# Optimization experiments

Measured on AMD Instinct MI355X. Metric: run time of the kernel, lower is better.

Reference implementation:

```python
import jax, jax.numpy as jnp
import numpy as np

HID, DSTATE, K, DIN, HDIM, NH, CHUNK = 2048, 128, 4, 4096, 64, 64, 256
CONVD = DIN + 2 * DSTATE  # 4352
EPS = 1e-5


def setup_inputs() -> dict:
    key = jax.random.key(0)
    ks = jax.random.split(key, 10)
    B, L = 2, 4096
    hidden_states = jax.random.normal(ks[0], (B, L, HID), jnp.float32)
    proj_out = 2 * (DIN + DSTATE) + NH  # 8512
    in_proj_w = jax.random.normal(ks[1], (proj_out, HID), jnp.float32) * (HID ** -0.5)
    conv_w = jax.random.normal(ks[2], (CONVD, K), jnp.float32) * (K ** -0.5)
    conv_b = jax.random.normal(ks[3], (CONVD,), jnp.float32) * 0.01
    dt_bias = jax.random.uniform(ks[4], (NH,), jnp.float32)
    A = jax.random.uniform(ks[5], (NH,), jnp.float32, minval=1.0, maxval=16.0)
    A_log = jnp.log(A)
    D = jnp.ones((NH,), jnp.float32)
    norm_w = jnp.ones((DIN,), jnp.float32)
    out_proj_w = jax.random.normal(ks[6], (HID, DIN), jnp.float32) * (DIN ** -0.5)
    return {"hidden_states": hidden_states, "in_proj_w": in_proj_w, "conv_w": conv_w,
            "conv_b": conv_b, "dt_bias": dt_bias, "A_log": A_log, "D": D,
            "norm_w": norm_w, "out_proj_w": out_proj_w}


def _segsum(x):
    # x: [..., L] -> [..., L, L] lower-triangular cumulative sums, -inf above diag
    Lc = x.shape[-1]
    cs = jnp.cumsum(x, -1)
    seg = cs[..., :, None] - cs[..., None, :]
    mask = jnp.tril(jnp.ones((Lc, Lc), bool))
    return jnp.where(mask, seg, -jnp.inf)


def _causal_conv1d(x, w, b):
    # x: [B, L, D] depthwise causal conv, kernel K, then SiLU
    L = x.shape[1]
    xp = jnp.pad(x, ((0, 0), (K - 1, 0), (0, 0)))
    y = sum(xp[:, i:i + L, :] * w[:, i] for i in range(K)) + b
    return jax.nn.silu(y)


def _ssd(x, Bm, Cm, dt, A, D):
    # x:[b,l,h,p]  Bm,Cm:[b,l,n]  dt:[b,l,h] (post-softplus)  A:[h]  D:[h]
    b, l, h, p = x.shape
    n = Bm.shape[-1]
    c = l // CHUNK
    xr = x.reshape(b, c, CHUNK, h, p)
    Br = Bm.reshape(b, c, CHUNK, n)
    Cr = Cm.reshape(b, c, CHUNK, n)
    dtr = dt.reshape(b, c, CHUNK, h)
    Adt = jnp.transpose(dtr * A, (0, 3, 1, 2))          # [b,h,c,L]
    Acs = jnp.cumsum(Adt, -1)                            # [b,h,c,L]
    Lmat = jnp.exp(_segsum(Adt))                         # [b,h,c,L,L]
    xdt = xr * dtr[..., None]                            # [b,c,L,h,p]
    # intra-chunk (diagonal) term
    Yd = jnp.einsum('bcln,bcsn,bhcls,bcshp->bclhp', Cr, Br, Lmat, xdt)
    # per-chunk final states
    decay_states = jnp.exp(Acs[..., -1:] - Acs)          # [b,h,c,L]
    chunk_states = jnp.einsum('bcln,bhcl,bclhp->bchpn', Br, decay_states, xdt)
    chunk_decay = jnp.exp(Acs[..., -1])                  # [b,h,c]
    def step(state, inp):
        dec, cs = inp
        return state * dec[..., None, None] + cs, state
    init = jnp.zeros((b, h, p, n), x.dtype)
    _, prev = jax.lax.scan(step, init,
                           (jnp.moveaxis(chunk_decay, -1, 0), jnp.moveaxis(chunk_states, 1, 0)))
    prev = jnp.moveaxis(prev, 0, 1)                      # [b,c,h,p,n] state entering each chunk
    Yo = jnp.einsum('bcln,bchpn,bhcl->bclhp', Cr, prev, jnp.exp(Acs))
    Y = Yd + Yo + xr * D[:, None]
    return Y.reshape(b, l, h * p)


def _gated_rmsnorm(y, z, w):
    y32 = y.astype(jnp.float32) * jax.nn.silu(z.astype(jnp.float32))
    var = jnp.mean(y32 * y32, -1, keepdims=True)
    return (y32 * jax.lax.rsqrt(var + EPS) * w).astype(y.dtype)


def reference(hidden_states, in_proj_w, conv_w, conv_b, dt_bias, A_log, D, norm_w, out_proj_w):
    zxbcdt = hidden_states @ in_proj_w.T                 # [b,l,8512]
    z = zxbcdt[..., :DIN]
    xBC = zxbcdt[..., DIN:DIN + CONVD]
    dt = zxbcdt[..., DIN + CONVD:]                       # [b,l,h]
    xBC = _causal_conv1d(xBC, conv_w, conv_b)
    x = xBC[..., :DIN]
    Bm = xBC[..., DIN:DIN + DSTATE]
    Cm = xBC[..., DIN + DSTATE:]
    A = -jnp.exp(A_log)
    dt = jax.nn.softplus(dt + dt_bias)
    b, l, _ = x.shape
    y = _ssd(x.reshape(b, l, NH, HDIM), Bm, Cm, dt, A, D)
    y = _gated_rmsnorm(y, z, norm_w)
    return y @ out_proj_w.T
```

## Files before the change

kernel.cpp:

```cpp
#include <hip/hip_runtime.h>
#include <hip/hip_bf16.h>


typedef __bf16 v8bf __attribute__((ext_vector_type(8)));
typedef float  v4f  __attribute__((ext_vector_type(4)));

#define LL long long

__device__ inline v8bf load8(const float* p) {
    v4f a = *(const v4f*)p, b = *(const v4f*)(p + 4);
    v8bf r;
#pragma unroll
    for (int i = 0; i < 4; ++i) { r[i] = (__bf16)a[i]; r[i + 4] = (__bf16)b[i]; }
    return r;
}

__device__ __forceinline__ void gload_lds16(const __bf16* g, __bf16* l) {
    __builtin_amdgcn_global_load_lds(
        (const __attribute__((address_space(1))) void*)g,
        (__attribute__((address_space(3))) void*)l, 16, 0, 0);
}

__global__ __launch_bounds__(256) void cast_bf16_kernel(
    const float* __restrict__ in, __bf16* __restrict__ out)
{
    LL i = ((LL)blockIdx.x * 256 + threadIdx.x) * 8;
    *(v8bf*)&out[i] = load8(&in[i]);
}

__global__ __launch_bounds__(256) void cast_split_kernel(
    const float* __restrict__ in, __bf16* __restrict__ hi,
    __bf16* __restrict__ lo)
{
    LL i = ((LL)blockIdx.x * 256 + threadIdx.x) * 8;
    v4f a = *(const v4f*)&in[i], b = *(const v4f*)&in[i + 4];
    v8bf h, l;
#pragma unroll
    for (int k = 0; k < 4; ++k) {
        __bf16 hh = (__bf16)a[k];  h[k]     = hh;  l[k]     = (__bf16)(a[k] - (float)hh);
        __bf16 hb = (__bf16)b[k];  h[k + 4] = hb;  l[k + 4] = (__bf16)(b[k] - (float)hb);
    }
    *(v8bf*)&hi[i] = h;
    *(v8bf*)&lo[i] = l;
}

template <int MODE, int TM, int TN, int RN>
__global__ __launch_bounds__(512, 2) void gemm_bt_8p(
    const __bf16* __restrict__ Ab, const __bf16* __restrict__ Bb, int KT,
    int lda, int ldb,
    __bf16* __restrict__ z_out, __bf16* __restrict__ x_out,
    float* __restrict__ outf, int ldc)
{
    __shared__ __align__(16) __bf16 lds[65536];
    constexpr int RM = 8 / RN;
    constexpr int LM = TM / RM, LN = TN / RN;
    const int orig = blockIdx.x;
    const int x = orig & 7, loc = orig >> 3;
    const int M0 = ((x / RN) * LM + loc / LN) * 256;
    const int N0 = ((x % RN) * LN + loc % LN) * 256;

    const int tid  = threadIdx.x;
    const int lane = tid & 63, wave = tid >> 6;
    const int wr = wave >> 2, wc = wave & 3;
    const int lrow = lane & 15, quad = lane >> 4;
    const int row0 = tid >> 3;
    const int g0   = (tid & 7) ^ (row0 & 7);

    v4f acc[8][4] = {};
    v8bf aF[2][4], b0F[2][2], b1F[2][2];

#define STAGE_A(par, half, kt) do { \
    const __bf16* _s = Ab + (size_t)(M0 + (half)*128 + row0) * lda + (kt)*64 + g0*8; \
    __bf16* _d = lds + ((par)*2 + (half)) * 8192 + wave * 512; \
    gload_lds16(_s, _d); \
    gload_lds16(_s + (size_t)64 * lda, _d + 4096); \
} while (0)

#define STAGE_B(par, half, kt) do { \
    const __bf16* _s = Bb + (size_t)(N0 + (half)*128 + row0) * ldb + (kt)*64 + g0*8; \
    __bf16* _d = lds + 32768 + ((par)*2 + (half)) * 8192 + wave * 512; \
    gload_lds16(_s, _d); \
    gload_lds16(_s + (size_t)64 * ldb, _d + 4096); \
} while (0)

#define READ_A(par, qm) do { \
    const __bf16* _s = lds + ((par)*2 + wr) * 8192; \
    _Pragma("unroll") \
    for (int _ks = 0; _ks < 2; ++_ks) \
      _Pragma("unroll") \
      for (int _m = 0; _m < 4; ++_m) \
        aF[_ks][_m] = *(const v8bf*)&_s[((qm)*64 + _m*16 + lrow)*64 + \
                                        ((((_ks<<2)+quad) ^ (lrow&7))<<3)]; \
} while (0)

#define READ_B(par, qn, DST) do { \
    const __bf16* _s = lds + 32768 + ((par)*2 + (wc>>1)) * 8192; \
    _Pragma("unroll") \
    for (int _ks = 0; _ks < 2; ++_ks) \
      _Pragma("unroll") \
      for (int _n = 0; _n < 2; ++_n) \
        DST[_ks][_n] = *(const v8bf*)&_s[((wc&1)*64 + (qn)*32 + _n*16 + lrow)*64 + \
                                         ((((_ks<<2)+quad) ^ (lrow&7))<<3)]; \
} while (0)

#define MFQ(qm, qn, BF) do { \
    __builtin_amdgcn_s_setprio(1); \
    _Pragma("unroll") \
    for (int _ks = 0; _ks < 2; ++_ks) \
      _Pragma("unroll") \
      for (int _m = 0; _m < 4; ++_m) \
        _Pragma("unroll") \
        for (int _n = 0; _n < 2; ++_n) \
          acc[(qm)*4+_m][(qn)*2+_n] = __builtin_amdgcn_mfma_f32_16x16x32_bf16( \
              aF[_ks][_m], BF[_ks][_n], acc[(qm)*4+_m][(qn)*2+_n], 0, 0, 0); \
    __builtin_amdgcn_s_setprio(0); \
} while (0)

#define PBAR  __builtin_amdgcn_s_barrier()
#define LGKM0 asm volatile("s_waitcnt lgkmcnt(0)" ::: "memory")
#define VMC4  asm volatile("s_waitcnt vmcnt(4)" ::: "memory")
#define VMC0  asm volatile("s_waitcnt vmcnt(0)" ::: "memory")

    STAGE_A(0, 0, 0); STAGE_A(0, 1, 0); STAGE_B(0, 0, 0); STAGE_B(0, 1, 0);
    STAGE_A(1, 0, 1); STAGE_B(1, 0, 1);
    VMC4; PBAR;

    const int KT2 = KT >> 1;
    for (int it = 0; it < KT2; ++it) {
        const int T0 = 2 * it, T1 = 2 * it + 1;
        const bool notlast = (it < KT2 - 1);
        READ_A(0, 0); READ_B(0, 0, b0F);
        STAGE_A(1, 1, T1);
        PBAR; LGKM0; MFQ(0, 0, b0F); PBAR;
        READ_B(0, 1, b1F);
        STAGE_B(1, 1, T1);
        PBAR; LGKM0; MFQ(0, 1, b1F); PBAR;
        READ_A(0, 1);
        if (notlast) STAGE_B(0, 0, T0 + 2);
        PBAR; LGKM0; MFQ(1, 0, b0F); PBAR;
        if (notlast) STAGE_A(0, 0, T0 + 2);
        PBAR; LGKM0; MFQ(1, 1, b1F);
        if (notlast) { VMC4; } else { VMC0; }
        PBAR;
        READ_A(1, 0); READ_B(1, 0, b0F);
        if (notlast) STAGE_A(0, 1, T0 + 2);
        PBAR; LGKM0; MFQ(0, 0, b0F); PBAR;
        READ_B(1, 1, b1F);
        if (notlast) STAGE_B(0, 1, T0 + 2);
        PBAR; LGKM0; MFQ(0, 1, b1F); PBAR;
        READ_A(1, 1);
        if (notlast) STAGE_B(1, 0, T1 + 2);
        PBAR; LGKM0; MFQ(1, 0, b0F); PBAR;
        if (notlast) STAGE_A(1, 0, T1 + 2);
        PBAR; LGKM0; MFQ(1, 1, b1F);
        if (notlast) { VMC4; } else { VMC0; }
        PBAR;
    }

#undef STAGE_A
#undef STAGE_B
#undef READ_A
#undef READ_B
#undef MFQ

#pragma unroll
    for (int m = 0; m < 8; ++m)
#pragma unroll
        for (int n = 0; n < 4; ++n)
#pragma unroll
            for (int r = 0; r < 4; ++r) {
                int row = M0 + wr * 128 + m * 16 + quad * 4 + r;
                int col = N0 + wc * 64 + n * 16 + lrow;
                float v = acc[m][n][r];
                if constexpr (MODE == 1) {
                    if (col < 4096) z_out[(LL)row * 4096 + col] = (__bf16)v;
                    else            x_out[(LL)row * 4096 + (col - 4096)] = (__bf16)v;
                } else {
                    outf[(LL)row * ldc + col] = v;
                }
            }
}

__global__ __launch_bounds__(256) void bcdt_gemm_kernel(
    const __bf16* __restrict__ Ahi, const __bf16* __restrict__ Alo,
    const __bf16* __restrict__ Whi, const __bf16* __restrict__ Wlo,
    const float* __restrict__ dtbi,
    float* __restrict__ bcr, float* __restrict__ dt)
{
    __shared__ __align__(16) __bf16 sAh[128 * 64];
    __shared__ __align__(16) __bf16 sAl[128 * 64];
    __shared__ __align__(16) __bf16 sWh[64 * 64];
    __shared__ __align__(16) __bf16 sWl[64 * 64];
    const int orig = blockIdx.x;
    const int swz = (orig & 7) * 40 + (orig >> 3);
    const int m0 = (swz / 5) * 128;
    const int n0 = (swz % 5) * 64;
    const int tid = threadIdx.x;
    const int lane = tid & 63, wave = tid >> 6;
    const int lrow = lane & 15, quad = lane >> 4;
    const int wm = wave * 32;
    v4f acc[2][4] = {};

    for (int k0 = 0; k0 < 2048; k0 += 64) {
#pragma unroll
        for (int i = 0; i < 4; ++i) {
            int e = tid + i * 256;
            int row = e >> 3, g = (e & 7) ^ (row & 7);
            const LL so = (LL)(m0 + row) * 2048 + k0 + g * 8;
            gload_lds16(&Ahi[so], &sAh[wave * 512 + i * 2048]);
            gload_lds16(&Alo[so], &sAl[wave * 512 + i * 2048]);
        }
#pragma unroll
        for (int i = 0; i < 2; ++i) {
            int e = tid + i * 256;
            int row = e >> 3, g = (e & 7) ^ (row & 7);
            const LL so = (LL)(n0 + row) * 2048 + k0 + g * 8;
            gload_lds16(&Whi[so], &sWh[wave * 512 + i * 2048]);
            gload_lds16(&Wlo[so], &sWl[wave * 512 + i * 2048]);
        }
        __syncthreads();
#pragma unroll
        for (int ks = 0; ks < 2; ++ks) {
            v8bf ah[2], al[2], wh[4], wl[4];
#pragma unroll
            for (int i = 0; i < 2; ++i) {
                int r = wm + i * 16 + lrow;
                int c = ((((ks << 2) + quad) ^ (lrow & 7)) << 3);
                ah[i] = *(const v8bf*)&sAh[r * 64 + c];
                al[i] = *(const v8bf*)&sAl[r * 64 + c];
            }
#pragma unroll
            for (int j = 0; j < 4; ++j) {
                int r = j * 16 + lrow;
                int c = ((((ks << 2) + quad) ^ (lrow & 7)) << 3);
                wh[j] = *(const v8bf*)&sWh[r * 64 + c];
                wl[j] = *(const v8bf*)&sWl[r * 64 + c];
            }
#pragma unroll
            for (int i = 0; i < 2; ++i)
#pragma unroll
                for (int j = 0; j < 4; ++j) {
                    acc[i][j] = __builtin_amdgcn_mfma_f32_16x16x32_bf16(ah[i], wh[j], acc[i][j], 0, 0, 0);
                    acc[i][j] = __builtin_amdgcn_mfma_f32_16x16x32_bf16(ah[i], wl[j], acc[i][j], 0, 0, 0);
                    acc[i][j] = __builtin_amdgcn_mfma_f32_16x16x32_bf16(al[i], wh[j], acc[i][j], 0, 0, 0);
                }
        }
        __syncthreads();
    }
#pragma unroll
    for (int i = 0; i < 2; ++i)
#pragma unroll
        for (int j = 0; j < 4; ++j)
#pragma unroll
            for (int r = 0; r < 4; ++r) {
                int row = m0 + wm + i * 16 + quad * 4 + r;
                int sc = n0 + j * 16 + lrow;
                float v = acc[i][j][r];
                if (sc < 256) {
                    bcr[(LL)row * 256 + sc] = v;
                } else {
                    float x = v + dtbi[sc - 256];
                    dt[row * 64 + (sc - 256)] = (x > 20.f) ? x : log1pf(__expf(x));
                }
            }
}

__global__ __launch_bounds__(256) void conv_x_kernel(
    const __bf16* __restrict__ xp, const float* __restrict__ cw,
    const float* __restrict__ cbias, __bf16* __restrict__ xq)
{
    int ch = blockIdx.x * 256 + threadIdx.x;
    int l = blockIdx.y, b = blockIdx.z;
    float acc = cbias[ch];
#pragma unroll
    for (int i = 0; i < 4; ++i) {
        int ls = l - 3 + i;
        if (ls >= 0)
            acc += (float)xp[((LL)b * 4096 + ls) * 4096 + ch] * cw[ch * 4 + i];
    }
    acc = acc / (1.f + __expf(-acc));
    xq[((LL)b * 4096 + l) * 4096 + ch] = (__bf16)acc;
}

__global__ __launch_bounds__(256) void conv_bc_kernel(
    const float* __restrict__ bcr, const float* __restrict__ cw,
    const float* __restrict__ cbias, float* __restrict__ bcc)
{
    int ch = threadIdx.x;
    int l = blockIdx.y, b = blockIdx.z;
    float acc = cbias[4096 + ch];
#pragma unroll
    for (int i = 0; i < 4; ++i) {
        int ls = l - 3 + i;
        if (ls >= 0)
            acc += bcr[((LL)b * 4096 + ls) * 256 + ch] * cw[(4096 + ch) * 4 + i];
    }
    acc = acc / (1.f + __expf(-acc));
    bcc[((LL)b * 4096 + l) * 256 + ch] = acc;
}

__global__ __launch_bounds__(256) void cumsum_kernel(
    const float* __restrict__ dt, const float* __restrict__ alog,
    float* __restrict__ acs, float* __restrict__ cdec)
{
    int h = blockIdx.x, c = blockIdx.y, b = blockIdx.z;
    int s = threadIdx.x;
    __shared__ float buf[256];
    float Av = -expf(alog[h]);
    int bl = b * 4096 + c * 256 + s;
    buf[s] = dt[bl * 64 + h] * Av;
    __syncthreads();
    for (int off = 1; off < 256; off <<= 1) {
        float v = (s >= off) ? buf[s - off] : 0.f;
        __syncthreads();
        buf[s] += v;
        __syncthreads();
    }
    int abase = (((b * 16) + c) * 64 + h) * 256;
    acs[abase + s] = buf[s];
    if (s == 255) cdec[(b * 64 + h) * 16 + c] = expf(buf[s]);
}

__global__ __launch_bounds__(256) void chunk_state_kernel(
    const __bf16* __restrict__ xq, const float* __restrict__ bcc,
    const float* __restrict__ dtb, const float* __restrict__ acs,
    float* __restrict__ cs)
{
    int h = blockIdx.x, c = blockIdx.y, b = blockIdx.z;
    int t = threadIdx.x;
    int lg = t & 63, pg = t >> 6;
    int n0 = lg * 2;
    __shared__ __align__(16) float xdt_s[64 * 68];
    __shared__ float dec_s[64];
    const LL lbase = (LL)b * 4096 + c * 256;
    const int abase = (((b * 16) + c) * 64 + h) * 256;
    float alast = acs[abase + 255];
    float a0[16] = {}, a1[16] = {};
    for (int st = 0; st < 4; ++st) {
        for (int i = 0; i < 16; ++i) {
            int e = t + i * 256; int sp = e >> 6, p = e & 63;
            LL row = lbase + st * 64 + sp;
            xdt_s[sp * 68 + p] = (float)xq[row * 4096 + h * 64 + p] * dtb[(row << 6) + h];
        }
        if (t < 64) dec_s[t] = __expf(alast - acs[abase + st * 64 + t]);
        __syncthreads();
        for (int sp = 0; sp < 64; ++sp) {
            LL row = lbase + st * 64 + sp;
            float2 bb = *(const float2*)&bcc[row * 256 + n0];
            float dd = dec_s[sp];
            float b0 = bb.x * dd, b1 = bb.y * dd;
#pragma unroll
            for (int q = 0; q < 4; ++q) {
                v4f xv = *(const v4f*)&xdt_s[sp * 68 + pg * 16 + q * 4];
#pragma unroll
                for (int j = 0; j < 4; ++j) { a0[q * 4 + j] += b0 * xv[j]; a1[q * 4 + j] += b1 * xv[j]; }
            }
        }
        __syncthreads();
    }
    const LL obase = ((LL)(((b * 16) + c) * 64 + h)) * 8192;
    for (int pp = 0; pp < 16; ++pp) {
        int p = pg * 16 + pp;
        cs[obase + p * 128 + n0]     = a0[pp];
        cs[obase + p * 128 + n0 + 1] = a1[pp];
    }
}

__global__ __launch_bounds__(256) void scan_kernel(
    float* __restrict__ cs, const float* __restrict__ cdec)
{
    int h = blockIdx.x, b = blockIdx.y;
    int t = threadIdx.x;
    float st[32];
#pragma unroll
    for (int i = 0; i < 32; ++i) st[i] = 0.f;
    for (int c = 0; c < 16; ++c) {
        LL base = ((LL)(((b * 16) + c) * 64 + h)) * 8192;
        float cd = cdec[(b * 64 + h) * 16 + c];
#pragma unroll
        for (int i = 0; i < 32; ++i) {
            int e = i * 256 + t;
            float v = cs[base + e];
            cs[base + e] = st[i];
            st[i] = st[i] * cd + v;
        }
    }
}

__global__ __launch_bounds__(256) void cb_kernel(const float* __restrict__ bcc,
                                                 float* __restrict__ cbt)
{
    int st = blockIdx.x, c = blockIdx.y, b = blockIdx.z;
    int t = threadIdx.x;
    int lg = t & 63, pg = t >> 6;
    __shared__ float cr_s[256 * 33];
    __shared__ __align__(16) float brT[32 * 68];
    const LL lbase = (LL)b * 4096 + c * 256;
    float acc[4][16] = {};
    for (int nt = 0; nt < 4; ++nt) {
        for (int i = 0; i < 32; ++i) {
            int e = t + i * 256; int l = e >> 5, np = e & 31;
            cr_s[l * 33 + np] = bcc[(lbase + l) * 256 + 128 + nt * 32 + np];
        }
        for (int i = 0; i < 8; ++i) {
            int e = t + i * 256; int sp = e >> 5, np = e & 31;
            brT[np * 68 + sp] = bcc[(lbase + st * 64 + sp) * 256 + nt * 32 + np];
        }
        __syncthreads();
        for (int np = 0; np < 32; ++np) {
            float w0 = cr_s[lg * 33 + np],         w1 = cr_s[(lg + 64) * 33 + np];
            float w2 = cr_s[(lg + 128) * 33 + np], w3 = cr_s[(lg + 192) * 33 + np];
#pragma unroll
            for (int q = 0; q < 4; ++q) {
                v4f bv = *(const v4f*)&brT[np * 68 + pg * 16 + q * 4];
#pragma unroll
                for (int j = 0; j < 4; ++j) {
                    acc[0][q * 4 + j] += w0 * bv[j]; acc[1][q * 4 + j] += w1 * bv[j];
                    acc[2][q * 4 + j] += w2 * bv[j]; acc[3][q * 4 + j] += w3 * bv[j];
                }
            }
        }
        __syncthreads();
    }
    const LL obase = ((LL)((b * 16) + c)) * 65536;
#pragma unroll
    for (int r = 0; r < 4; ++r)
        for (int sp = 0; sp < 16; ++sp) {
            int s = st * 64 + pg * 16 + sp;
            cbt[obase + (LL)s * 256 + (lg + r * 64)] = acc[r][sp];
        }
}

__global__ __launch_bounds__(256) void ssd_y_kernel(
    __bf16* __restrict__ xq, const float* __restrict__ bcc,
    const float* __restrict__ dtb, const float* __restrict__ acs,
    const float* __restrict__ cbt, const float* __restrict__ prevS,
    const float* __restrict__ Dv)
{
    const int h = blockIdx.x, c = blockIdx.y, b = blockIdx.z;
    const int t = threadIdx.x;
    const int lane = t & 63, wave = t >> 6;
    const int lrow = lane & 15, quad = lane >> 4;
    const int wm = wave * 64;
    __shared__ __align__(16) __bf16 As[256][72];
    __shared__ __align__(16) __bf16 Bs[64 * 64];
    __shared__ float acs_s[256];
    const LL lbase = (LL)b * 4096 + c * 256;
    const int abase = (((b * 16) + c) * 64 + h) * 256;
    acs_s[t] = acs[abase + t];
    __syncthreads();
    const float acl_t = acs_s[t];
    const float ea_t  = __expf(acl_t);
    const LL cbbase = ((LL)((b * 16) + c)) * 65536;
    const LL pbase  = ((LL)(((b * 16) + c) * 64 + h)) * 8192;
    v4f acc[4][4] = {};

    for (int kb = 0; kb < 6; ++kb) {
        if (kb < 4) {
            const int sb = kb * 64;
#pragma unroll
            for (int g = 0; g < 8; ++g) {
                v8bf wv;
#pragma unroll
                for (int u = 0; u < 8; ++u) {
                    int s = sb + g * 8 + u;
                    float cbv = cbt[cbbase + (LL)s * 256 + t];
                    float d = acl_t - acs_s[s];
                    wv[u] = (__bf16)((s <= t) ? cbv * __expf(d) : 0.f);
                }
                *(v8bf*)&As[t][g * 8] = wv;
            }
        } else {
            const int nb = (kb - 4) * 64;
            const LL cb0 = (lbase + t) * 256 + 128 + nb;
#pragma unroll
            for (int g = 0; g < 8; ++g) {
                v4f c0 = *(const v4f*)&bcc[cb0 + g * 8];
                v4f c1 = *(const v4f*)&bcc[cb0 + g * 8 + 4];
                v8bf wv;
#pragma unroll
                for (int u = 0; u < 4; ++u) {
                    wv[u]     = (__bf16)(c0[u] * ea_t);
                    wv[u + 4] = (__bf16)(c1[u] * ea_t);
                }
                *(v8bf*)&As[t][g * 8] = wv;
            }
        }
        if (kb < 4) {
            const int sb = kb * 64;
#pragma unroll
            for (int i = 0; i < 16; ++i) {
                int e = t + i * 256; int p = e & 63, sp = e >> 6;
                LL row = lbase + sb + sp;
                float xv = (float)xq[row * 4096 + h * 64 + p] * dtb[((int)(row)) * 64 + h];
                Bs[p * 64 + ((((sp >> 3) ^ (p & 7)) << 3) | (sp & 7))] = (__bf16)xv;
            }
        } else {
            const int nb = (kb - 4) * 64;
#pragma unroll
            for (int i = 0; i < 16; ++i) {
                int e = t + i * 256; int n = e & 63, p = e >> 6;
                float pv = prevS[pbase + (LL)p * 128 + nb + n];
                Bs[p * 64 + ((((n >> 3) ^ (p & 7)) << 3) | (n & 7))] = (__bf16)pv;
            }
        }
        __syncthreads();
#pragma unroll
        for (int ks = 0; ks < 2; ++ks) {
            v8bf af[4], bfv[4];
#pragma unroll
            for (int i = 0; i < 4; ++i)
                af[i] = *(const v8bf*)&As[wm + i * 16 + lrow][ks * 32 + quad * 8];
#pragma unroll
            for (int j = 0; j < 4; ++j) {
                int p = j * 16 + lrow;
                int kg = (ks * 4 + quad) ^ (p & 7);
                bfv[j] = *(const v8bf*)&Bs[p * 64 + kg * 8];
            }
#pragma unroll
            for (int i = 0; i < 4; ++i)
#pragma unroll
                for (int j = 0; j < 4; ++j)
                    acc[i][j] = __builtin_amdgcn_mfma_f32_16x16x32_bf16(af[i], bfv[j], acc[i][j], 0, 0, 0);
        }
        __syncthreads();
    }
    const float Dh = Dv[h];
#pragma unroll
    for (int i = 0; i < 4; ++i)
#pragma unroll
        for (int j = 0; j < 4; ++j)
#pragma unroll
            for (int r = 0; r < 4; ++r) {
                int l = wm + i * 16 + quad * 4 + r;
                int p = j * 16 + lrow;
                LL idx = (lbase + l) * 4096 + h * 64 + p;
                float v = acc[i][j][r] + Dh * (float)xq[idx];
                xq[idx] = (__bf16)v;
            }
}

__global__ __launch_bounds__(256) void rmsnorm_kernel(
    __bf16* __restrict__ y, const __bf16* __restrict__ z,
    const float* __restrict__ nw)
{
    LL r = blockIdx.x;
    int t = threadIdx.x;
    float vals[16]; float ss = 0.f;
#pragma unroll
    for (int i = 0; i < 16; ++i) {
        int j = i * 256 + t;
        float yv = (float)y[r * 4096 + j];
        float zv = (float)z[r * 4096 + j];
        float v = yv * (zv / (1.f + __expf(-zv)));
        vals[i] = v; ss += v * v;
    }
#pragma unroll
    for (int off = 32; off >= 1; off >>= 1) ss += __shfl_down(ss, off, 64);
    __shared__ float red[4];
    if ((t & 63) == 0) red[t >> 6] = ss;
    __syncthreads();
    float tot = red[0] + red[1] + red[2] + red[3];
    float rstd = rsqrtf(tot * (1.f / 4096.f) + 1e-5f);
#pragma unroll
    for (int i = 0; i < 16; ++i) {
        int j = i * 256 + t;
        y[r * 4096 + j] = (__bf16)(vals[i] * rstd * nw[j]);
    }
}

extern "C" void kernel_launch(void* const* d_in, const int* in_sizes, int n_in,
                              void* d_out, int out_size, void* d_ws, size_t ws_size,
                              hipStream_t stream) {
    const float* hs    = (const float*)d_in[0];
    const float* w1    = (const float*)d_in[1];
    const float* cw    = (const float*)d_in[2];
    const float* cbias = (const float*)d_in[3];
    const float* dtbi  = (const float*)d_in[4];
    const float* alog  = (const float*)d_in[5];
    const float* Dv    = (const float*)d_in[6];
    const float* nw    = (const float*)d_in[7];
    const float* wo    = (const float*)d_in[8];
    float* out = (float*)d_out;
    (void)in_sizes; (void)n_in; (void)out_size; (void)ws_size;

    char* ws = (char*)d_ws;
    size_t off = 0;
    auto alloc = [&](size_t bytes) { void* p = ws + off; off += (bytes + 255) & ~(size_t)255; return p; };
    __bf16* xp_b  = (__bf16*)alloc((size_t)8192 * 4096 * 2);
    __bf16* xq_b  = (__bf16*)alloc((size_t)8192 * 4096 * 2);
    float*  bcr_f = (float*) alloc((size_t)8192 * 256 * 4);
    float*  bcc_f = (float*) alloc((size_t)8192 * 256 * 4);
    float*  dt_f  = (float*) alloc((size_t)8192 * 64 * 4);
    float*  acs_f = (float*) alloc((size_t)2 * 16 * 64 * 256 * 4);
    float*  cd_f  = (float*) alloc((size_t)2 * 64 * 16 * 4);
    float*  cbt_f = (float*) alloc((size_t)2 * 16 * 256 * 256 * 4);
    float*  cs_f  = (float*)xp_b;
    __bf16* z_b   = (__bf16*)d_out;

    __bf16* hs_b  = xq_b;
    __bf16* w1_b  = xq_b + (size_t)8192 * 2048;
    __bf16* hs_lo = (__bf16*)xp_b;
    __bf16* ws_hi = hs_lo + (size_t)8192 * 2048;
    __bf16* ws_lo = ws_hi + (size_t)320 * 2048;
    __bf16* wo_b  = (__bf16*)xp_b;

    cast_split_kernel<<<8192, 256, 0, stream>>>(hs, hs_b, hs_lo);
    cast_bf16_kernel<<<8192, 256, 0, stream>>>(w1, w1_b);
    cast_split_kernel<<<320, 256, 0, stream>>>(w1 + (size_t)8192 * 2048, ws_hi, ws_lo);
    bcdt_gemm_kernel<<<320, 256, 0, stream>>>(hs_b, hs_lo, ws_hi, ws_lo,
                                              dtbi, bcr_f, dt_f);
    gemm_bt_8p<1, 32, 32, 4><<<dim3(1024), 512, 0, stream>>>(
        hs_b, w1_b, 32, 2048, 2048, z_b, xp_b, nullptr, 0);
    conv_x_kernel<<<dim3(16, 4096, 2), 256, 0, stream>>>(xp_b, cw, cbias, xq_b);
    conv_bc_kernel<<<dim3(1, 4096, 2), 256, 0, stream>>>(bcr_f, cw, cbias, bcc_f);
    cumsum_kernel<<<dim3(64, 16, 2), 256, 0, stream>>>(dt_f, alog, acs_f, cd_f);
    chunk_state_kernel<<<dim3(64, 16, 2), 256, 0, stream>>>(xq_b, bcc_f, dt_f, acs_f, cs_f);
    scan_kernel<<<dim3(64, 2), 256, 0, stream>>>(cs_f, cd_f);
    cb_kernel<<<dim3(4, 16, 2), 256, 0, stream>>>(bcc_f, cbt_f);
    ssd_y_kernel<<<dim3(64, 16, 2), 256, 0, stream>>>(xq_b, bcc_f, dt_f, acs_f, cbt_f, cs_f, Dv);
    cast_bf16_kernel<<<4096, 256, 0, stream>>>(wo, wo_b);
    rmsnorm_kernel<<<8192, 256, 0, stream>>>(xq_b, z_b, nw);
    gemm_bt_8p<2, 32, 8, 1><<<dim3(256), 512, 0, stream>>>(
        xq_b, wo_b, 64, 4096, 4096, nullptr, nullptr, out, 2048);
}
```

Measured before the change: 1.389 ms.

## Skip causal-zero tiles in SSD diag term and split CB kernel rows

The intra-chunk term of the SSD output kernel now skips MFMA work for waves whose row block lies entirely above the causal diagonal. Off-diagonal tiles get their decay weights from a factored exp (row factor times a per-column factor in shared memory) instead of one exp per element, so only diagonal tiles compute full pairwise exps. The C-scaling fill is remapped to coalesced loads through a shared exp buffer. The CB kernel is split into twice as many blocks, each covering half the rows, to raise parallelism. In exchange the code adds more branching and an explicit waitcnt/sched barrier, and the factored exp may slightly change rounding.

```diff
diff --git a/kernel.cpp b/kernel.cpp
--- a/kernel.cpp
+++ b/kernel.cpp
@@ -390,17 +390,20 @@
 __global__ __launch_bounds__(256) void cb_kernel(const float* __restrict__ bcc,
                                                  float* __restrict__ cbt)
 {
-    int st = blockIdx.x, c = blockIdx.y, b = blockIdx.z;
+    int bx = blockIdx.x;
+    int st = bx & 3, lh = bx >> 2;
+    int c = blockIdx.y, b = blockIdx.z;
     int t = threadIdx.x;
     int lg = t & 63, pg = t >> 6;
-    __shared__ float cr_s[256 * 33];
+    __shared__ float cr_s[128 * 33];
     __shared__ __align__(16) float brT[32 * 68];
     const LL lbase = (LL)b * 4096 + c * 256;
-    float acc[4][16] = {};
+    const int l0 = lh * 128;
+    float acc[2][16] = {};
     for (int nt = 0; nt < 4; ++nt) {
-        for (int i = 0; i < 32; ++i) {
+        for (int i = 0; i < 16; ++i) {
             int e = t + i * 256; int l = e >> 5, np = e & 31;
-            cr_s[l * 33 + np] = bcc[(lbase + l) * 256 + 128 + nt * 32 + np];
+            cr_s[l * 33 + np] = bcc[(lbase + l0 + l) * 256 + 128 + nt * 32 + np];
         }
         for (int i = 0; i < 8; ++i) {
             int e = t + i * 256; int sp = e >> 5, np = e & 31;
@@ -408,15 +411,14 @@
         }
         __syncthreads();
         for (int np = 0; np < 32; ++np) {
-            float w0 = cr_s[lg * 33 + np],         w1 = cr_s[(lg + 64) * 33 + np];
-            float w2 = cr_s[(lg + 128) * 33 + np], w3 = cr_s[(lg + 192) * 33 + np];
+            float w0 = cr_s[lg * 33 + np], w1 = cr_s[(lg + 64) * 33 + np];
 #pragma unroll
             for (int q = 0; q < 4; ++q) {
                 v4f bv = *(const v4f*)&brT[np * 68 + pg * 16 + q * 4];
 #pragma unroll
                 for (int j = 0; j < 4; ++j) {
-                    acc[0][q * 4 + j] += w0 * bv[j]; acc[1][q * 4 + j] += w1 * bv[j];
-                    acc[2][q * 4 + j] += w2 * bv[j]; acc[3][q * 4 + j] += w3 * bv[j];
+                    acc[0][q * 4 + j] += w0 * bv[j];
+                    acc[1][q * 4 + j] += w1 * bv[j];
                 }
             }
         }
@@ -424,10 +426,10 @@
     }
     const LL obase = ((LL)((b * 16) + c)) * 65536;
 #pragma unroll
-    for (int r = 0; r < 4; ++r)
+    for (int r = 0; r < 2; ++r)
         for (int sp = 0; sp < 16; ++sp) {
             int s = st * 64 + pg * 16 + sp;
-            cbt[obase + (LL)s * 256 + (lg + r * 64)] = acc[r][sp];
+            cbt[obase + (LL)s * 256 + (l0 + lg + r * 64)] = acc[r][sp];
         }
 }
 
@@ -445,12 +447,14 @@
     __shared__ __align__(16) __bf16 As[256][72];
     __shared__ __align__(16) __bf16 Bs[64 * 64];
     __shared__ float acs_s[256];
+    __shared__ float ea_s[256];
+    __shared__ float qbuf[64];
     const LL lbase = (LL)b * 4096 + c * 256;
     const int abase = (((b * 16) + c) * 64 + h) * 256;
     acs_s[t] = acs[abase + t];
+    const float acl_t = acs_s[t];
+    ea_s[t] = __expf(acl_t);
     __syncthreads();
-    const float acl_t = acs_s[t];
-    const float ea_t  = __expf(acl_t);
     const LL cbbase = ((LL)((b * 16) + c)) * 65536;
     const LL pbase  = ((LL)(((b * 16) + c) * 64 + h)) * 8192;
     v4f acc[4][4] = {};
@@ -458,45 +462,49 @@
     for (int kb = 0; kb < 6; ++kb) {
         if (kb < 4) {
             const int sb = kb * 64;
-#pragma unroll
-            for (int g = 0; g < 8; ++g) {
-                v8bf wv;
-#pragma unroll
-                for (int u = 0; u < 8; ++u) {
-                    int s = sb + g * 8 + u;
-                    float cbv = cbt[cbbase + (LL)s * 256 + t];
-                    float d = acl_t - acs_s[s];
-                    wv[u] = (__bf16)((s <= t) ? cbv * __expf(d) : 0.f);
-                }
-                *(v8bf*)&As[t][g * 8] = wv;
-            }
-        } else {
-            const int nb = (kb - 4) * 64;
-            const LL cb0 = (lbase + t) * 256 + 128 + nb;
-#pragma unroll
-            for (int g = 0; g < 8; ++g) {
-                v4f c0 = *(const v4f*)&bcc[cb0 + g * 8];
-                v4f c1 = *(const v4f*)&bcc[cb0 + g * 8 + 4];
-                v8bf wv;
-#pragma unroll
-                for (int u = 0; u < 4; ++u) {
-                    wv[u]     = (__bf16)(c0[u] * ea_t);
-                    wv[u + 4] = (__bf16)(c1[u] * ea_t);
-                }
-                *(v8bf*)&As[t][g * 8] = wv;
-            }
-        }
-        if (kb < 4) {
-            const int sb = kb * 64;
+            if (t < 64) qbuf[t] = __expf(acs_s[sb + 63] - acs_s[sb + t]);
+            {
+                const int row = sb + wave * 16 + lrow;
+                const int c0 = quad * 16;
+                const float al = acs_s[row];
+                v8bf wv0, wv1;
+#pragma unroll
+                for (int j = 0; j < 8; ++j) {
+                    int s0 = sb + c0 + j;
+                    int s1 = s0 + 8;
+                    float cb0 = cbt[cbbase + (LL)s0 * 256 + row];
+                    float cb1 = cbt[cbbase + (LL)s1 * 256 + row];
+                    wv0[j] = (__bf16)((s0 <= row) ? cb0 * __expf(al - acs_s[s0]) : 0.f);
+                    wv1[j] = (__bf16)((s1 <= row) ? cb1 * __expf(al - acs_s[s1]) : 0.f);
+                }
+                *(v8bf*)&As[row][c0]     = wv0;
+                *(v8bf*)&As[row][c0 + 8] = wv1;
+            }
 #pragma unroll
             for (int i = 0; i < 16; ++i) {
                 int e = t + i * 256; int p = e & 63, sp = e >> 6;
                 LL row = lbase + sb + sp;
-                float xv = (float)xq[row * 4096 + h * 64 + p] * dtb[((int)(row)) * 64 + h];
+                float xv = (float)xq[row * 4096 + h * 64 + p] * dtb[((int)row) * 64 + h];
                 Bs[p * 64 + ((((sp >> 3) ^ (p & 7)) << 3) | (sp & 7))] = (__bf16)xv;
             }
         } else {
             const int nb = (kb - 4) * 64;
+#pragma unroll
+            for (int i = 0; i < 8; ++i) {
+                int e = t + i * 256;
+                int l = e >> 3, g = e & 7;
+                const LL cb0 = (lbase + l) * 256 + 128 + nb + g * 8;
+                v4f c0 = *(const v4f*)&bcc[cb0];
+                v4f c1 = *(const v4f*)&bcc[cb0 + 4];
+                float ea = ea_s[l];
+                v8bf wv;
+#pragma unroll
+                for (int u = 0; u < 4; ++u) {
+                    wv[u]     = (__bf16)(c0[u] * ea);
+                    wv[u + 4] = (__bf16)(c1[u] * ea);
+                }
+                *(v8bf*)&As[l][g * 8] = wv;
+            }
 #pragma unroll
             for (int i = 0; i < 16; ++i) {
                 int e = t + i * 256; int n = e & 63, p = e >> 6;
@@ -505,23 +513,45 @@
             }
         }
         __syncthreads();
-#pragma unroll
-        for (int ks = 0; ks < 2; ++ks) {
-            v8bf af[4], bfv[4];
-#pragma unroll
-            for (int i = 0; i < 4; ++i)
-                af[i] = *(const v8bf*)&As[wm + i * 16 + lrow][ks * 32 + quad * 8];
-#pragma unroll
-            for (int j = 0; j < 4; ++j) {
-                int p = j * 16 + lrow;
-                int kg = (ks * 4 + quad) ^ (p & 7);
-                bfv[j] = *(const v8bf*)&Bs[p * 64 + kg * 8];
-            }
-#pragma unroll
-            for (int i = 0; i < 4; ++i)
-#pragma unroll
-                for (int j = 0; j < 4; ++j)
-                    acc[i][j] = __builtin_amdgcn_mfma_f32_16x16x32_bf16(af[i], bfv[j], acc[i][j], 0, 0, 0);
+        if (kb < 4 && wave > kb) {
+            const int sb = kb * 64;
+            const float r = __expf(acl_t - acs_s[sb + 63]);
+#pragma unroll
+            for (int g = 0; g < 8; ++g) {
+                v4f q0 = *(const v4f*)&qbuf[g * 8];
+                v4f q1 = *(const v4f*)&qbuf[g * 8 + 4];
+                v8bf wv;
+#pragma unroll
+                for (int u = 0; u < 4; ++u) {
+                    float cbv0 = cbt[cbbase + (LL)(sb + g * 8 + u) * 256 + t];
+                    float cbv1 = cbt[cbbase + (LL)(sb + g * 8 + 4 + u) * 256 + t];
+                    wv[u]     = (__bf16)(cbv0 * (r * q0[u]));
+                    wv[u + 4] = (__bf16)(cbv1 * (r * q1[u]));
+                }
+                *(v8bf*)&As[t][g * 8] = wv;
+            }
+            asm volatile("s_waitcnt lgkmcnt(0)" ::: "memory");
+            __builtin_amdgcn_sched_barrier(0);
+        }
+        if (kb >= 4 || wave >= kb) {
+#pragma unroll
+            for (int ks = 0; ks < 2; ++ks) {
+                v8bf af[4], bfv[4];
+#pragma unroll
+                for (int i = 0; i < 4; ++i)
+                    af[i] = *(const v8bf*)&As[wm + i * 16 + lrow][ks * 32 + quad * 8];
+#pragma unroll
+                for (int j = 0; j < 4; ++j) {
+                    int p = j * 16 + lrow;
+                    int kg = (ks * 4 + quad) ^ (p & 7);
+                    bfv[j] = *(const v8bf*)&Bs[p * 64 + kg * 8];
+                }
+#pragma unroll
+                for (int i = 0; i < 4; ++i)
+#pragma unroll
+                    for (int j = 0; j < 4; ++j)
+                        acc[i][j] = __builtin_amdgcn_mfma_f32_16x16x32_bf16(af[i], bfv[j], acc[i][j], 0, 0, 0);
+            }
         }
         __syncthreads();
     }
@@ -617,7 +647,7 @@
     cumsum_kernel<<<dim3(64, 16, 2), 256, 0, stream>>>(dt_f, alog, acs_f, cd_f);
     chunk_state_kernel<<<dim3(64, 16, 2), 256, 0, stream>>>(xq_b, bcc_f, dt_f, acs_f, cs_f);
     scan_kernel<<<dim3(64, 2), 256, 0, stream>>>(cs_f, cd_f);
-    cb_kernel<<<dim3(4, 16, 2), 256, 0, stream>>>(bcc_f, cbt_f);
+    cb_kernel<<<dim3(8, 16, 2), 256, 0, stream>>>(bcc_f, cbt_f);
     ssd_y_kernel<<<dim3(64, 16, 2), 256, 0, stream>>>(xq_b, bcc_f, dt_f, acs_f, cbt_f, cs_f, Dv);
     cast_bf16_kernel<<<4096, 256, 0, stream>>>(wo, wo_b);
     rmsnorm_kernel<<<8192, 256, 0, stream>>>(xq_b, z_b, nw);
```

Measured after the change: 1.644 ms. 1.18x slower.

## Skip upper-triangular tiles in SSD intra-chunk and factor decay exponentials

Applied to the files above, without the earlier changes.

ssd_y_kernel now skips building and multiplying the strictly upper-triangular 64-row tiles per wave, since the causal mask zeroes them. Fully-below-diagonal tiles compute the decay as a product of a per-row and per-column exponential, which replaces a per-element exp. cb_kernel splits rows across twice as many blocks for more parallelism. This introduces wave-dependent branches inside the loop and a small numerical change from the factored exponentials.

```diff
diff --git a/kernel.cpp b/kernel.cpp
--- a/kernel.cpp
+++ b/kernel.cpp
@@ -390,17 +390,20 @@
 __global__ __launch_bounds__(256) void cb_kernel(const float* __restrict__ bcc,
                                                  float* __restrict__ cbt)
 {
-    int st = blockIdx.x, c = blockIdx.y, b = blockIdx.z;
+    int bx = blockIdx.x;
+    int st = bx & 3, lh = bx >> 2;
+    int c = blockIdx.y, b = blockIdx.z;
     int t = threadIdx.x;
     int lg = t & 63, pg = t >> 6;
-    __shared__ float cr_s[256 * 33];
+    __shared__ float cr_s[128 * 33];
     __shared__ __align__(16) float brT[32 * 68];
     const LL lbase = (LL)b * 4096 + c * 256;
-    float acc[4][16] = {};
+    const int l0 = lh * 128;
+    float acc[2][16] = {};
     for (int nt = 0; nt < 4; ++nt) {
-        for (int i = 0; i < 32; ++i) {
+        for (int i = 0; i < 16; ++i) {
             int e = t + i * 256; int l = e >> 5, np = e & 31;
-            cr_s[l * 33 + np] = bcc[(lbase + l) * 256 + 128 + nt * 32 + np];
+            cr_s[l * 33 + np] = bcc[(lbase + l0 + l) * 256 + 128 + nt * 32 + np];
         }
         for (int i = 0; i < 8; ++i) {
             int e = t + i * 256; int sp = e >> 5, np = e & 31;
@@ -408,15 +411,14 @@
         }
         __syncthreads();
         for (int np = 0; np < 32; ++np) {
-            float w0 = cr_s[lg * 33 + np],         w1 = cr_s[(lg + 64) * 33 + np];
-            float w2 = cr_s[(lg + 128) * 33 + np], w3 = cr_s[(lg + 192) * 33 + np];
+            float w0 = cr_s[lg * 33 + np], w1 = cr_s[(lg + 64) * 33 + np];
 #pragma unroll
             for (int q = 0; q < 4; ++q) {
                 v4f bv = *(const v4f*)&brT[np * 68 + pg * 16 + q * 4];
 #pragma unroll
                 for (int j = 0; j < 4; ++j) {
-                    acc[0][q * 4 + j] += w0 * bv[j]; acc[1][q * 4 + j] += w1 * bv[j];
-                    acc[2][q * 4 + j] += w2 * bv[j]; acc[3][q * 4 + j] += w3 * bv[j];
+                    acc[0][q * 4 + j] += w0 * bv[j];
+                    acc[1][q * 4 + j] += w1 * bv[j];
                 }
             }
         }
@@ -424,10 +426,10 @@
     }
     const LL obase = ((LL)((b * 16) + c)) * 65536;
 #pragma unroll
-    for (int r = 0; r < 4; ++r)
+    for (int r = 0; r < 2; ++r)
         for (int sp = 0; sp < 16; ++sp) {
             int s = st * 64 + pg * 16 + sp;
-            cbt[obase + (LL)s * 256 + (lg + r * 64)] = acc[r][sp];
+            cbt[obase + (LL)s * 256 + (l0 + lg + r * 64)] = acc[r][sp];
         }
 }
 
@@ -445,12 +447,15 @@
     __shared__ __align__(16) __bf16 As[256][72];
     __shared__ __align__(16) __bf16 Bs[64 * 64];
     __shared__ float acs_s[256];
+    __shared__ float qbuf[4][64];
     const LL lbase = (LL)b * 4096 + c * 256;
     const int abase = (((b * 16) + c) * 64 + h) * 256;
     acs_s[t] = acs[abase + t];
     __syncthreads();
+    qbuf[t >> 6][t & 63] = __expf(acs_s[(t >> 6) * 64 + 63] - acs_s[t]);
     const float acl_t = acs_s[t];
     const float ea_t  = __expf(acl_t);
+    __syncthreads();
     const LL cbbase = ((LL)((b * 16) + c)) * 65536;
     const LL pbase  = ((LL)(((b * 16) + c) * 64 + h)) * 8192;
     v4f acc[4][4] = {};
@@ -458,17 +463,38 @@
     for (int kb = 0; kb < 6; ++kb) {
         if (kb < 4) {
             const int sb = kb * 64;
-#pragma unroll
-            for (int g = 0; g < 8; ++g) {
-                v8bf wv;
-#pragma unroll
-                for (int u = 0; u < 8; ++u) {
-                    int s = sb + g * 8 + u;
-                    float cbv = cbt[cbbase + (LL)s * 256 + t];
-                    float d = acl_t - acs_s[s];
-                    wv[u] = (__bf16)((s <= t) ? cbv * __expf(d) : 0.f);
-                }
-                *(v8bf*)&As[t][g * 8] = wv;
+            if (kb < wave) {
+                const float r = __expf(acl_t - acs_s[sb + 63]);
+#pragma unroll
+                for (int g = 0; g < 8; ++g) {
+                    v8bf wv;
+#pragma unroll
+                    for (int u = 0; u < 8; ++u) {
+                        float cbv = cbt[cbbase + (LL)(sb + g * 8 + u) * 256 + t];
+                        wv[u] = (__bf16)(cbv * (r * qbuf[kb][g * 8 + u]));
+                    }
+                    *(v8bf*)&As[t][g * 8] = wv;
+                }
+            } else if (kb == wave) {
+#pragma unroll
+                for (int g = 0; g < 8; ++g) {
+                    v8bf wv;
+#pragma unroll
+                    for (int u = 0; u < 8; ++u) {
+                        int s = sb + g * 8 + u;
+                        float cbv = cbt[cbbase + (LL)s * 256 + t];
+                        float d = acl_t - acs_s[s];
+                        wv[u] = (__bf16)((s <= t) ? cbv * __expf(d) : 0.f);
+                    }
+                    *(v8bf*)&As[t][g * 8] = wv;
+                }
+            }
+#pragma unroll
+            for (int i = 0; i < 16; ++i) {
+                int e = t + i * 256; int p = e & 63, sp = e >> 6;
+                LL row = lbase + sb + sp;
+                float xv = (float)xq[row * 4096 + h * 64 + p] * dtb[((int)row) * 64 + h];
+                Bs[p * 64 + ((((sp >> 3) ^ (p & 7)) << 3) | (sp & 7))] = (__bf16)xv;
             }
         } else {
             const int nb = (kb - 4) * 64;
@@ -485,18 +511,6 @@
                 }
                 *(v8bf*)&As[t][g * 8] = wv;
             }
-        }
-        if (kb < 4) {
-            const int sb = kb * 64;
-#pragma unroll
-            for (int i = 0; i < 16; ++i) {
-                int e = t + i * 256; int p = e & 63, sp = e >> 6;
-                LL row = lbase + sb + sp;
-                float xv = (float)xq[row * 4096 + h * 64 + p] * dtb[((int)(row)) * 64 + h];
-                Bs[p * 64 + ((((sp >> 3) ^ (p & 7)) << 3) | (sp & 7))] = (__bf16)xv;
-            }
-        } else {
-            const int nb = (kb - 4) * 64;
 #pragma unroll
             for (int i = 0; i < 16; ++i) {
                 int e = t + i * 256; int n = e & 63, p = e >> 6;
@@ -505,23 +519,25 @@
             }
         }
         __syncthreads();
-#pragma unroll
-        for (int ks = 0; ks < 2; ++ks) {
-            v8bf af[4], bfv[4];
-#pragma unroll
-            for (int i = 0; i < 4; ++i)
-                af[i] = *(const v8bf*)&As[wm + i * 16 + lrow][ks * 32 + quad * 8];
-#pragma unroll
-            for (int j = 0; j < 4; ++j) {
-                int p = j * 16 + lrow;
-                int kg = (ks * 4 + quad) ^ (p & 7);
-                bfv[j] = *(const v8bf*)&Bs[p * 64 + kg * 8];
-            }
-#pragma unroll
-            for (int i = 0; i < 4; ++i)
-#pragma unroll
-                for (int j = 0; j < 4; ++j)
-                    acc[i][j] = __builtin_amdgcn_mfma_f32_16x16x32_bf16(af[i], bfv[j], acc[i][j], 0, 0, 0);
+        if (kb >= 4 || wave >= kb) {
+#pragma unroll
+            for (int ks = 0; ks < 2; ++ks) {
+                v8bf af[4], bfv[4];
+#pragma unroll
+                for (int i = 0; i < 4; ++i)
+                    af[i] = *(const v8bf*)&As[wm + i * 16 + lrow][ks * 32 + quad * 8];
+#pragma unroll
+                for (int j = 0; j < 4; ++j) {
+                    int p = j * 16 + lrow;
+                    int kg = (ks * 4 + quad) ^ (p & 7);
+                    bfv[j] = *(const v8bf*)&Bs[p * 64 + kg * 8];
+                }
+#pragma unroll
+                for (int i = 0; i < 4; ++i)
+#pragma unroll
+                    for (int j = 0; j < 4; ++j)
+                        acc[i][j] = __builtin_amdgcn_mfma_f32_16x16x32_bf16(af[i], bfv[j], acc[i][j], 0, 0, 0);
+            }
         }
         __syncthreads();
     }
@@ -617,7 +633,7 @@
     cumsum_kernel<<<dim3(64, 16, 2), 256, 0, stream>>>(dt_f, alog, acs_f, cd_f);
     chunk_state_kernel<<<dim3(64, 16, 2), 256, 0, stream>>>(xq_b, bcc_f, dt_f, acs_f, cs_f);
     scan_kernel<<<dim3(64, 2), 256, 0, stream>>>(cs_f, cd_f);
-    cb_kernel<<<dim3(4, 16, 2), 256, 0, stream>>>(bcc_f, cbt_f);
+    cb_kernel<<<dim3(8, 16, 2), 256, 0, stream>>>(bcc_f, cbt_f);
     ssd_y_kernel<<<dim3(64, 16, 2), 256, 0, stream>>>(xq_b, bcc_f, dt_f, acs_f, cbt_f, cs_f, Dv);
     cast_bf16_kernel<<<4096, 256, 0, stream>>>(wo, wo_b);
     rmsnorm_kernel<<<8192, 256, 0, stream>>>(xq_b, z_b, nw);
```

After: 1.458 ms. 1.05x slower.
